# Kernel optimization log

Measured on AMD Instinct MI355X. Metric: run time of the kernel, lower is better.

## Reference

```python
import jax, jax.numpy as jnp
import numpy as np

BND = 1.4

def setup_inputs() -> dict:
    key = jax.random.key(0)
    k1, k2 = jax.random.split(key)
    B, C = 8192, 32000
    output = jax.random.normal(k1, (B, C), dtype=jnp.float32)
    labels = jax.random.randint(k2, (B, 2), 0, 2, dtype=jnp.int64)
    return {"output": output, "labels": labels, "param_now": 0}

def reference(output, labels, param_now):
    # per-sample cross entropy (reduction='none')
    tag = labels[:, 0]                                   # [B] class indices
    abn = jnp.where(labels[:, 1] == 0, -1.0, 1.0)        # [B] in {-1, +1}
    logp = jax.nn.log_softmax(output, axis=-1)           # [B, C]
    ce = -jnp.take_along_axis(logp, tag[:, None], axis=-1)[:, 0]  # [B]
    # accumulate relu(BND - abn * loss) over the batch -> [1, 1]
    train_loss = jnp.sum(jax.nn.relu(BND - abn * ce))
    return train_loss.reshape(1, 1)
```

## Files before the change

### kernel.cpp

```cpp
#include <hip/hip_runtime.h>
#include <math.h>

#define BND 1.4f
#define L2E 1.44269504088896340736f
#define LN2 0.6931471805599453f

__global__ __launch_bounds__(256) void row_loss_kernel(
    const float* __restrict__ out,
    const int*   __restrict__ labels,
    float*       __restrict__ row_loss,
    int C) {
  const int row = blockIdx.x;
  const float4* __restrict__ rowp = (const float4*)(out + (size_t)row * C);
  const int n4 = C >> 2;

  float s = 0.f;
  for (int j = threadIdx.x; j < n4; j += 256) {
    float4 v = rowp[j];
    s += exp2f(v.x * L2E);
    s += exp2f(v.y * L2E);
    s += exp2f(v.z * L2E);
    s += exp2f(v.w * L2E);
  }

  #pragma unroll
  for (int off = 32; off > 0; off >>= 1)
    s += __shfl_down(s, off, 64);

  __shared__ float wsum[4];
  const int lane = threadIdx.x & 63;
  const int wave = threadIdx.x >> 6;
  if (lane == 0) wsum[wave] = s;
  __syncthreads();

  if (threadIdx.x == 0) {
    float tot = wsum[0] + wsum[1] + wsum[2] + wsum[3];
    int tag = labels[row * 2 + 0];
    int ab  = labels[row * 2 + 1];
    float abn = (ab == 0) ? -1.f : 1.f;
    float xt = out[(size_t)row * C + tag];
    float ce = LN2 * log2f(tot) - xt;
    row_loss[row] = fmaxf(BND - abn * ce, 0.f);
  }
}

__global__ __launch_bounds__(256) void reduce_kernel(
    const float* __restrict__ rl, float* __restrict__ out, int n) {
  float s = 0.f;
  for (int i = threadIdx.x; i < n; i += 256) s += rl[i];
  #pragma unroll
  for (int off = 32; off > 0; off >>= 1)
    s += __shfl_down(s, off, 64);
  __shared__ float wsum[4];
  const int lane = threadIdx.x & 63;
  const int wave = threadIdx.x >> 6;
  if (lane == 0) wsum[wave] = s;
  __syncthreads();
  if (threadIdx.x == 0) out[0] = wsum[0] + wsum[1] + wsum[2] + wsum[3];
}

extern "C" void kernel_launch(void* const* d_in, const int* in_sizes, int n_in,
                              void* d_out, int out_size, void* d_ws, size_t ws_size,
                              hipStream_t stream) {
  const float* output = (const float*)d_in[0];
  const int*   labels = (const int*)d_in[1];

  const int B = in_sizes[1] / 2;
  const int C = in_sizes[0] / B;

  float* row_loss = (float*)d_ws;

  row_loss_kernel<<<B, 256, 0, stream>>>(output, labels, row_loss, C);
  reduce_kernel<<<1, 256, 0, stream>>>(row_loss, (float*)d_out, B);
}
```

Before: 1.296 ms.

## Exit rows early when a partial exp-sum bound already zeroes the hinge

For rows whose label flag is 1, the kernel sums exp over the first 4096 logits, then checks the total against twice exp(BND + x_tag). Because the exp-sum only grows as more logits are added, exceeding that threshold means the cross entropy is above BND and the relu is zero. Those rows write 0 and skip reading the rest of the row. The main loop also gets four independent accumulators, and the final reduce loads float4. In exchange it adds a block-wide sync and branch, and it assumes C is at least 4096 and that B and C are multiples of 4.

```diff
diff --git a/kernel.cpp b/kernel.cpp
--- a/kernel.cpp
+++ b/kernel.cpp
@@ -5,58 +5,89 @@
 #define L2E 1.44269504088896340736f
 #define LN2 0.6931471805599453f
 
+__device__ __forceinline__ float esum4(float4 v) {
+  return (exp2f(v.x * L2E) + exp2f(v.y * L2E)) +
+         (exp2f(v.z * L2E) + exp2f(v.w * L2E));
+}
+
 __global__ __launch_bounds__(256) void row_loss_kernel(
     const float* __restrict__ out,
     const int*   __restrict__ labels,
     float*       __restrict__ row_loss,
     int C) {
   const int row = blockIdx.x;
-  const float4* __restrict__ rowp = (const float4*)(out + (size_t)row * C);
+  const float*  __restrict__ rp   = out + (size_t)row * C;
+  const float4* __restrict__ rowp = (const float4*)rp;
   const int n4 = C >> 2;
+  const int t  = threadIdx.x;
+  const int lane = t & 63, wave = t >> 6;
 
-  float s = 0.f;
-  for (int j = threadIdx.x; j < n4; j += 256) {
-    float4 v = rowp[j];
-    s += exp2f(v.x * L2E);
-    s += exp2f(v.y * L2E);
-    s += exp2f(v.z * L2E);
-    s += exp2f(v.w * L2E);
+  const int tag = labels[row * 2 + 0];
+  const int ab  = labels[row * 2 + 1];
+  const float xt = rp[tag];
+
+  __shared__ float wsum[4];
+  __shared__ int early;
+
+  float s0 = esum4(rowp[t]);
+  float s1 = esum4(rowp[t + 256]);
+  float s2 = esum4(rowp[t + 512]);
+  float s3 = esum4(rowp[t + 768]);
+
+  if (ab != 0) {
+    float p = (s0 + s1) + (s2 + s3);
+    #pragma unroll
+    for (int off = 32; off > 0; off >>= 1) p += __shfl_down(p, off, 64);
+    if (lane == 0) wsum[wave] = p;
+    __syncthreads();
+    if (t == 0) {
+      float tot1 = wsum[0] + wsum[1] + wsum[2] + wsum[3];
+      float thr  = 2.f * exp2f((BND + xt) * L2E);
+      early = (tot1 > thr) ? 1 : 0;
+      if (early) row_loss[row] = 0.f;
+    }
+    __syncthreads();
+    if (early) return;
   }
 
+  int j = t + 1024;
+  for (; j + 768 < n4; j += 1024) {
+    s0 += esum4(rowp[j]);
+    s1 += esum4(rowp[j + 256]);
+    s2 += esum4(rowp[j + 512]);
+    s3 += esum4(rowp[j + 768]);
+  }
+  for (; j < n4; j += 256) s0 += esum4(rowp[j]);
+
+  float s = (s0 + s1) + (s2 + s3);
   #pragma unroll
-  for (int off = 32; off > 0; off >>= 1)
-    s += __shfl_down(s, off, 64);
+  for (int off = 32; off > 0; off >>= 1) s += __shfl_down(s, off, 64);
+  if (lane == 0) wsum[wave] = s;
+  __syncthreads();
+  if (t == 0) {
+    float tot = wsum[0] + wsum[1] + wsum[2] + wsum[3];
+    float abn = (ab == 0) ? -1.f : 1.f;
+    float ce  = LN2 * log2f(tot) - xt;
+    row_loss[row] = fmaxf(BND - abn * ce, 0.f);
+  }
+}
 
+__global__ __launch_bounds__(256) void reduce_kernel(
+    const float* __restrict__ rl, float* __restrict__ outp, int n) {
+  const float4* __restrict__ r4 = (const float4*)rl;
+  float s = 0.f;
+  for (int i = threadIdx.x; i < (n >> 2); i += 256) {
+    float4 v = r4[i];
+    s += (v.x + v.y) + (v.z + v.w);
+  }
+  #pragma unroll
+  for (int off = 32; off > 0; off >>= 1) s += __shfl_down(s, off, 64);
   __shared__ float wsum[4];
   const int lane = threadIdx.x & 63;
   const int wave = threadIdx.x >> 6;
   if (lane == 0) wsum[wave] = s;
   __syncthreads();
-
-  if (threadIdx.x == 0) {
-    float tot = wsum[0] + wsum[1] + wsum[2] + wsum[3];
-    int tag = labels[row * 2 + 0];
-    int ab  = labels[row * 2 + 1];
-    float abn = (ab == 0) ? -1.f : 1.f;
-    float xt = out[(size_t)row * C + tag];
-    float ce = LN2 * log2f(tot) - xt;
-    row_loss[row] = fmaxf(BND - abn * ce, 0.f);
-  }
-}
-
-__global__ __launch_bounds__(256) void reduce_kernel(
-    const float* __restrict__ rl, float* __restrict__ out, int n) {
-  float s = 0.f;
-  for (int i = threadIdx.x; i < n; i += 256) s += rl[i];
-  #pragma unroll
-  for (int off = 32; off > 0; off >>= 1)
-    s += __shfl_down(s, off, 64);
-  __shared__ float wsum[4];
-  const int lane = threadIdx.x & 63;
-  const int wave = threadIdx.x >> 6;
-  if (lane == 0) wsum[wave] = s;
-  __syncthreads();
-  if (threadIdx.x == 0) out[0] = wsum[0] + wsum[1] + wsum[2] + wsum[3];
+  if (threadIdx.x == 0) outp[0] = wsum[0] + wsum[1] + wsum[2] + wsum[3];
 }
 
 extern "C" void kernel_launch(void* const* d_in, const int* in_sizes, int n_in,
```

After: 1.218 ms. 6.0% less time.
